# Optimization experiments

Measured on AMD Instinct MI355X. Metric: run time of the kernel, lower is better.

The kernel has to match this reference:

```python
import jax, jax.numpy as jnp
import numpy as np

EPS = 1e-6

def _log(t):
    return jnp.log(t + EPS)

def setup_inputs() -> dict:
    key = jax.random.key(0)
    k1, k2, k3 = jax.random.split(key, 3)
    b, h, n, d, k = 8, 12, 1024, 64, 256
    attn = jax.random.uniform(k1, (b, h, n, n), dtype=jnp.float32)
    attn = attn / jnp.sum(attn, axis=-1, keepdims=True)  # softmax-like rows
    value = jax.random.normal(k2, (b, h, n, d), dtype=jnp.float32)
    mask = jnp.ones((b, n), dtype=bool)
    # uniform noise for gumbel sampling, kept away from {0,1} for stability
    gumbel_u = jax.random.uniform(k3, (b, k, n - 1), dtype=jnp.float32,
                                  minval=1e-6, maxval=1.0 - 1e-6)
    return {"attn": attn, "value": value, "mask": mask,
            "gumbel_u": gumbel_u, "output_num_tokens": k}

def reference(attn, value, mask, gumbel_u, output_num_tokens):
    b, h, n, _ = attn.shape
    # cls-token attention to all other tokens, weighted by value norms
    cls_attn = attn[:, :, 0, 1:]                                  # [b,h,n-1]
    value_norms = jnp.linalg.norm(value[:, :, 1:, :], axis=-1)    # [b,h,n-1]
    cls_attn = jnp.einsum('bhn,bhn->bn', cls_attn, value_norms)   # [b,n-1]
    normed = cls_attn / (jnp.sum(cls_attn, axis=-1, keepdims=True) + EPS)
    pseudo_logits = _log(normed)
    mask_without_cls = mask[:, 1:]
    mask_value = -jnp.finfo(attn.dtype).max / 2
    pseudo_logits = jnp.where(~mask_without_cls, mask_value, pseudo_logits)
    # gumbel-max sampling: k independent draws per batch row
    gumbel = -_log(-_log(gumbel_u))                               # [b,k,n-1]
    sampled = jnp.argmax(pseudo_logits[:, None, :] + gumbel, axis=-1) + 1  # [b,k]
    # fixed-shape unique+sort: sort, zero-out duplicates, re-sort (zeros pre-pad)
    s = jnp.sort(sampled, axis=-1)
    dup = jnp.concatenate([jnp.zeros((b, 1), bool), s[:, 1:] == s[:, :-1]], axis=-1)
    uniq = jnp.sort(jnp.where(dup, 0, s), axis=-1)                # [b,k], zeros in front
    ids = jnp.pad(uniq, ((0, 0), (1, 0)))                          # prepend cls idx 0
    new_mask = jnp.pad(uniq != 0, ((0, 0), (1, 0)), constant_values=True)
    # gather selected rows of attn along token axis
    new_attn = jnp.take_along_axis(attn, ids[:, None, :, None], axis=2)  # [b,h,k+1,n]
    return new_attn, new_mask, ids
```

## Files before the change

kernel.cpp:

```cpp
#include <hip/hip_runtime.h>
#include <cfloat>
#include <cmath>

#define EPS 1e-6f

constexpr int B = 8, H = 12, N = 1024, D = 64, K = 256;
constexpr int NM1 = N - 1;
constexpr int KP1 = K + 1;

__global__ __launch_bounds__(256) void k1_cls(const float* __restrict__ attn,
                                              const float* __restrict__ value,
                                              float* __restrict__ cls) {
    int wave = (blockIdx.x * blockDim.x + threadIdx.x) >> 6;
    int lane = threadIdx.x & 63;
    if (wave >= B * NM1) return;
    int b = wave / NM1;
    int j = wave - b * NM1;
    float acc = 0.f;
    for (int h = 0; h < H; ++h) {
        const float* vrow = value + (((size_t)(b * H + h) * N) + (1 + j)) * D;
        float v = vrow[lane];
        float ss = v * v;
        #pragma unroll
        for (int off = 32; off > 0; off >>= 1)
            ss += __shfl_xor(ss, off, 64);
        float nrm = sqrtf(ss);
        float a = attn[(size_t)(b * H + h) * N * N + 1 + j];
        acc += a * nrm;
    }
    if (lane == 0) cls[b * NM1 + j] = acc;
}

__global__ __launch_bounds__(256) void k2_logits(float* __restrict__ cls,
                                                 const int* __restrict__ mask) {
    int b = blockIdx.x;
    int tid = threadIdx.x;
    __shared__ float red[256];
    float s = 0.f;
    for (int j = tid; j < NM1; j += 256) s += cls[b * NM1 + j];
    red[tid] = s;
    __syncthreads();
    for (int off = 128; off > 0; off >>= 1) {
        if (tid < off) red[tid] += red[tid + off];
        __syncthreads();
    }
    float denom = red[0] + EPS;
    const float mask_value = -(FLT_MAX * 0.5f);
    for (int j = tid; j < NM1; j += 256) {
        float pl = logf(cls[b * NM1 + j] / denom + EPS);
        if (mask[b * N + 1 + j] == 0) pl = mask_value;
        cls[b * NM1 + j] = pl;
    }
}

__global__ __launch_bounds__(256) void k3_sample(const float* __restrict__ logits,
                                                 const float* __restrict__ gu,
                                                 int* __restrict__ sampled) {
    int wave = (blockIdx.x * blockDim.x + threadIdx.x) >> 6;
    int lane = threadIdx.x & 63;
    if (wave >= B * K) return;
    int b = wave / K;
    int k = wave - b * K;
    const float* u  = gu + (size_t)(b * K + k) * NM1;
    const float* lg = logits + b * NM1;
    float best = -FLT_MAX;
    int bestj = 0x7fffffff;
    for (int j = lane; j < NM1; j += 64) {
        float g = -logf(-logf(u[j] + EPS) + EPS);
        float v = lg[j] + g;
        if (v > best) { best = v; bestj = j; }
    }
    #pragma unroll
    for (int off = 32; off > 0; off >>= 1) {
        float ov = __shfl_xor(best, off, 64);
        int   oj = __shfl_xor(bestj, off, 64);
        if (ov > best || (ov == best && oj < bestj)) { best = ov; bestj = oj; }
    }
    if (lane == 0) sampled[b * K + k] = bestj + 1;
}

__global__ __launch_bounds__(256) void k4_sort(const int* __restrict__ sampled,
                                               int* __restrict__ ws_ids,
                                               float* __restrict__ out_ids,
                                               float* __restrict__ out_mask) {
    int b = blockIdx.x;
    int tid = threadIdx.x;
    __shared__ int s[K];
    __shared__ int sc[K];
    __shared__ int uniq[K];
    s[tid] = sampled[b * K + tid];
    for (int size = 2; size <= K; size <<= 1) {
        for (int stride = size >> 1; stride > 0; stride >>= 1) {
            __syncthreads();
            int partner = tid ^ stride;
            if (partner > tid) {
                bool asc = ((tid & size) == 0);
                int a = s[tid], c = s[partner];
                if ((a > c) == asc) { s[tid] = c; s[partner] = a; }
            }
        }
    }
    __syncthreads();
    int v = s[tid];
    int flag = (tid == 0) ? 1 : ((v != s[tid - 1]) ? 1 : 0);
    sc[tid] = flag;
    for (int off = 1; off < K; off <<= 1) {
        __syncthreads();
        int add = (tid >= off) ? sc[tid - off] : 0;
        __syncthreads();
        sc[tid] += add;
    }
    __syncthreads();
    int total = sc[K - 1];
    int nz = K - total;
    uniq[tid] = 0;
    __syncthreads();
    if (flag) uniq[nz + sc[tid] - 1] = v;
    __syncthreads();
    int idv = uniq[tid];
    ws_ids[b * KP1 + 1 + tid]   = idv;
    out_ids[b * KP1 + 1 + tid]  = (float)idv;
    out_mask[b * KP1 + 1 + tid] = idv ? 1.0f : 0.0f;
    if (tid == 0) {
        ws_ids[b * KP1]   = 0;
        out_ids[b * KP1]  = 0.0f;
        out_mask[b * KP1] = 1.0f;
    }
}

__global__ __launch_bounds__(256) void k5_gather(const float* __restrict__ attn,
                                                 const int* __restrict__ ids,
                                                 float* __restrict__ out) {
    int row = blockIdx.x;
    int bh = row / KP1;
    int t = row - bh * KP1;
    int b = bh / H;
    int id = ids[b * KP1 + t];
    const float4* src = (const float4*)(attn + ((size_t)bh * N + id) * N);
    float4* dst = (float4*)(out + (size_t)row * N);
    dst[threadIdx.x] = src[threadIdx.x];
}

extern "C" void kernel_launch(void* const* d_in, const int* in_sizes, int n_in,
                              void* d_out, int out_size, void* d_ws, size_t ws_size,
                              hipStream_t stream) {
    const float* attn  = (const float*)d_in[0];
    const float* value = (const float*)d_in[1];
    const int*   mask  = (const int*)d_in[2];
    const float* gu    = (const float*)d_in[3];

    float* out       = (float*)d_out;
    float* out_attn  = out;
    float* out_mask  = out + (size_t)B * H * KP1 * N;
    float* out_ids   = out_mask + B * KP1;

    float* ws_cls     = (float*)d_ws;
    int*   ws_sampled = (int*)(ws_cls + B * NM1);
    int*   ws_ids     = ws_sampled + B * K;

    k1_cls<<<(B * NM1 * 64 + 255) / 256, 256, 0, stream>>>(attn, value, ws_cls);
    k2_logits<<<B, 256, 0, stream>>>(ws_cls, mask);
    k3_sample<<<(B * K * 64 + 255) / 256, 256, 0, stream>>>(ws_cls, gu, ws_sampled);
    k4_sort<<<B, K, 0, stream>>>(ws_sampled, ws_ids, out_ids, out_mask);
    k5_gather<<<B * H * KP1, 256, 0, stream>>>(attn, ws_ids, out_attn);
}
```

Baseline: 533.5 us.

## Vectorize value-norm loads and fuse logit normalization into gumbel sampling

k1 now assigns four tokens per wave, with 16 lanes each loading a float4 of the value row. This cuts the shuffle reduction depth and the number of waves. The separate logits kernel is folded into the sampling kernel: each block recomputes the per-batch sum and applies the log and mask inline. This removes one launch and one global round trip, at the cost of redundant denominator reductions and extra logf work per sample.

```diff
diff --git a/kernel.cpp b/kernel.cpp
--- a/kernel.cpp
+++ b/kernel.cpp
@@ -11,63 +11,58 @@
 __global__ __launch_bounds__(256) void k1_cls(const float* __restrict__ attn,
                                               const float* __restrict__ value,
                                               float* __restrict__ cls) {
-    int wave = (blockIdx.x * blockDim.x + threadIdx.x) >> 6;
+    int gtid = blockIdx.x * 256 + threadIdx.x;
+    int wave = gtid >> 6;
     int lane = threadIdx.x & 63;
-    if (wave >= B * NM1) return;
-    int b = wave / NM1;
-    int j = wave - b * NM1;
+    int q = wave * 4 + (lane >> 4);
+    int sub = lane & 15;
+    if (q >= B * NM1) return;
+    int b = q / NM1;
+    int j = q - b * NM1;
     float acc = 0.f;
     for (int h = 0; h < H; ++h) {
-        const float* vrow = value + (((size_t)(b * H + h) * N) + (1 + j)) * D;
-        float v = vrow[lane];
-        float ss = v * v;
-        #pragma unroll
-        for (int off = 32; off > 0; off >>= 1)
-            ss += __shfl_xor(ss, off, 64);
-        float nrm = sqrtf(ss);
+        const float4* vrow = (const float4*)(value + (((size_t)(b * H + h)) * N + 1 + j) * D);
+        float4 v = vrow[sub];
+        float ss = v.x * v.x + v.y * v.y + v.z * v.z + v.w * v.w;
+        ss += __shfl_xor(ss, 1, 64);
+        ss += __shfl_xor(ss, 2, 64);
+        ss += __shfl_xor(ss, 4, 64);
+        ss += __shfl_xor(ss, 8, 64);
         float a = attn[(size_t)(b * H + h) * N * N + 1 + j];
-        acc += a * nrm;
+        acc += a * sqrtf(ss);
     }
-    if (lane == 0) cls[b * NM1 + j] = acc;
+    if (sub == 0) cls[q] = acc;
 }
 
-__global__ __launch_bounds__(256) void k2_logits(float* __restrict__ cls,
-                                                 const int* __restrict__ mask) {
-    int b = blockIdx.x;
-    int tid = threadIdx.x;
+__global__ __launch_bounds__(256) void k23_sample(const float* __restrict__ cls,
+                                                  const int* __restrict__ mask,
+                                                  const float* __restrict__ gu,
+                                                  int* __restrict__ sampled) {
+    int b = blockIdx.x >> 6;
+    int k = ((blockIdx.x & 63) << 2) + (threadIdx.x >> 6);
+    int lane = threadIdx.x & 63;
+
     __shared__ float red[256];
     float s = 0.f;
-    for (int j = tid; j < NM1; j += 256) s += cls[b * NM1 + j];
-    red[tid] = s;
+    for (int j = threadIdx.x; j < NM1; j += 256) s += cls[b * NM1 + j];
+    red[threadIdx.x] = s;
     __syncthreads();
     for (int off = 128; off > 0; off >>= 1) {
-        if (tid < off) red[tid] += red[tid + off];
+        if (threadIdx.x < off) red[threadIdx.x] += red[threadIdx.x + off];
         __syncthreads();
     }
     float denom = red[0] + EPS;
     const float mask_value = -(FLT_MAX * 0.5f);
-    for (int j = tid; j < NM1; j += 256) {
-        float pl = logf(cls[b * NM1 + j] / denom + EPS);
-        if (mask[b * N + 1 + j] == 0) pl = mask_value;
-        cls[b * NM1 + j] = pl;
-    }
-}
 
-__global__ __launch_bounds__(256) void k3_sample(const float* __restrict__ logits,
-                                                 const float* __restrict__ gu,
-                                                 int* __restrict__ sampled) {
-    int wave = (blockIdx.x * blockDim.x + threadIdx.x) >> 6;
-    int lane = threadIdx.x & 63;
-    if (wave >= B * K) return;
-    int b = wave / K;
-    int k = wave - b * K;
     const float* u  = gu + (size_t)(b * K + k) * NM1;
-    const float* lg = logits + b * NM1;
+    const float* cb = cls + b * NM1;
     float best = -FLT_MAX;
     int bestj = 0x7fffffff;
     for (int j = lane; j < NM1; j += 64) {
+        float pl = logf(cb[j] / denom + EPS);
+        if (mask[b * N + 1 + j] == 0) pl = mask_value;
         float g = -logf(-logf(u[j] + EPS) + EPS);
-        float v = lg[j] + g;
+        float v = pl + g;
         if (v > best) { best = v; bestj = j; }
     }
     #pragma unroll
@@ -158,9 +153,8 @@
     int*   ws_sampled = (int*)(ws_cls + B * NM1);
     int*   ws_ids     = ws_sampled + B * K;
 
-    k1_cls<<<(B * NM1 * 64 + 255) / 256, 256, 0, stream>>>(attn, value, ws_cls);
-    k2_logits<<<B, 256, 0, stream>>>(ws_cls, mask);
-    k3_sample<<<(B * K * 64 + 255) / 256, 256, 0, stream>>>(ws_cls, gu, ws_sampled);
+    k1_cls<<<(B * NM1 / 4 * 64 + 255) / 256, 256, 0, stream>>>(attn, value, ws_cls);
+    k23_sample<<<B * (K / 4), 256, 0, stream>>>(ws_cls, mask, gu, ws_sampled);
     k4_sort<<<B, K, 0, stream>>>(ws_sampled, ws_ids, out_ids, out_mask);
     k5_gather<<<B * H * KP1, 256, 0, stream>>>(attn, ws_ids, out_attn);
 }
```

Result: no change. 531.2 us (-0.4%).
